# Kernel tuning notes

Measured on AMD Instinct MI355X. Metric: run time of the kernel, lower is better.

The kernel has to match this reference:

```python
import jax, jax.numpy as jnp
import numpy as np

T, H, E, I, K = 2048, 2048, 8, 1408, 2


def setup_inputs() -> dict:
    key = jax.random.key(0)
    k1, k2, k3, k4, k5 = jax.random.split(key, 5)
    s = 0.02
    return {
        "hidden_states": jax.random.normal(k1, (T, H), dtype=jnp.float32),
        "gate_w": jax.random.normal(k2, (E, H), dtype=jnp.float32) * s,   # router weight [n_experts, hidden]
        "w_gate": jax.random.normal(k3, (E, H, I), dtype=jnp.float32) * s,  # per-expert gate_proj
        "w_up": jax.random.normal(k4, (E, H, I), dtype=jnp.float32) * s,    # per-expert up_proj
        "w_down": jax.random.normal(k5, (E, I, H), dtype=jnp.float32) * s,  # per-expert down_proj
        "top_k": K,
    }


def reference(hidden_states, gate_w, w_gate, w_up, w_down, top_k):
    # Router: linear gate -> softmax -> top-k with renormalized weights (DeepSeek-V2 normal MoE)
    logits = hidden_states @ gate_w.T                       # [T, E]
    probs = jax.nn.softmax(logits, axis=-1)                 # [T, E]
    topv, topi = jax.lax.top_k(probs, top_k)                # [T, K]
    topv = topv / jnp.sum(topv, axis=-1, keepdims=True)     # norm_topk_prob
    nt, ne = probs.shape
    # Sparse combine weights [T, E] (zero for unselected experts)
    combine = jnp.zeros((nt, ne), probs.dtype).at[jnp.arange(nt)[:, None], topi].set(topv)
    # Expert MLPs (gated SiLU): down( silu(x @ Wg) * (x @ Wu) )
    g = jnp.einsum('th,ehi->tei', hidden_states, w_gate)    # [T, E, I]
    u = jnp.einsum('th,ehi->tei', hidden_states, w_up)
    a = jax.nn.silu(g) * u
    y = jnp.einsum('tei,eih->teh', a, w_down)               # [T, E, H]
    # Weighted combine over selected experts
    out = jnp.einsum('te,teh->th', combine, y)              # [T, H]
    return out
```

## Files before the change

kernel.cpp:

```cpp
#include <hip/hip_runtime.h>
#include <hip/hip_bf16.h>

#define T_TOK 2048
#define HID   2048
#define NEXP  8
#define INTER 1408

typedef float f32x4 __attribute__((ext_vector_type(4)));
typedef __bf16 bf16x8 __attribute__((ext_vector_type(8)));

__device__ __forceinline__ unsigned pk(__bf16 a, __bf16 b) {
    return (unsigned)__builtin_bit_cast(unsigned short, a) |
           ((unsigned)__builtin_bit_cast(unsigned short, b) << 16);
}

__global__ __launch_bounds__(256)
void router_kernel(const float* __restrict__ hs, const float* __restrict__ gw,
                   int* __restrict__ cnt, int* __restrict__ list,
                   float* __restrict__ wslot)
{
    const int wv = threadIdx.x >> 6, lane = threadIdx.x & 63;
    const int t = blockIdx.x * 4 + wv;
    float acc[8];
#pragma unroll
    for (int e = 0; e < 8; ++e) acc[e] = 0.f;
    const float* xr = hs + (size_t)t * HID;
    for (int it = 0; it < HID / 256; ++it) {
        const int h = it * 256 + lane * 4;
        float4 x = *reinterpret_cast<const float4*>(xr + h);
#pragma unroll
        for (int e = 0; e < 8; ++e) {
            float4 g = *reinterpret_cast<const float4*>(gw + e * HID + h);
            acc[e] += x.x * g.x + x.y * g.y + x.z * g.z + x.w * g.w;
        }
    }
#pragma unroll
    for (int e = 0; e < 8; ++e) {
#pragma unroll
        for (int off = 32; off >= 1; off >>= 1)
            acc[e] += __shfl_xor(acc[e], off, 64);
    }
    if (lane == 0) {
        int b0 = 0, b1 = -1;
        float v0 = -1e30f, v1 = -1e30f;
#pragma unroll
        for (int e = 0; e < 8; ++e) {
            if (acc[e] > v0) { v1 = v0; b1 = b0; v0 = acc[e]; b0 = e; }
            else if (acc[e] > v1) { v1 = acc[e]; b1 = e; }
        }
        float w0 = 1.f / (1.f + __expf(v1 - v0));
        float w1 = 1.f - w0;
        int p0 = atomicAdd(&cnt[b0], 1);
        list[b0 * T_TOK + p0] = 2 * t;
        wslot[2 * t] = w0;
        int p1 = atomicAdd(&cnt[b1], 1);
        list[b1 * T_TOK + p1] = 2 * t + 1;
        wslot[2 * t + 1] = w1;
    }
}

template<int MODE, int K_, int N_>
__global__ __launch_bounds__(256, 2)
void moe_gemm(const float* __restrict__ Asrc, const float* __restrict__ Ball,
              const int* __restrict__ cnt, const int* __restrict__ list,
              const float* __restrict__ wslot, const float* __restrict__ Gbuf,
              float* __restrict__ Obuf)
{
    const int e = blockIdx.z;
    const int cntE = cnt[e];
    const int rb = blockIdx.x * 128;
    if (rb >= cntE) return;
    const int nb = blockIdx.y * 128;
    const int tid = threadIdx.x;
    const int lane = tid & 63;
    const int wv = tid >> 6;
    const int wr = (wv >> 1) * 64, wc = (wv & 1) * 64;
    const int p = lane & 15, kg = lane >> 4;

    __shared__ __align__(16) __bf16 AhL[128 * 40], AlL[128 * 40];
    __shared__ __align__(16) __bf16 BhL[128 * 40], BlL[128 * 40];
    __shared__ int slots[128];

    if (tid < 128) {
        int r = rb + tid;
        slots[tid] = (r < cntE) ? list[e * T_TOK + r] : 0;
    }
    __syncthreads();

    const float* Bsrc = Ball + (size_t)e * K_ * N_;

    f32x4 acc[4][4];
#pragma unroll
    for (int i = 0; i < 4; ++i)
#pragma unroll
        for (int j = 0; j < 4; ++j) acc[i][j] = (f32x4)0.0f;

    for (int kt = 0; kt < K_ / 32; ++kt) {
        const int kb = kt * 32;
#pragma unroll
        for (int pp = 0; pp < 4; ++pp) {
            int idx = tid + pp * 256;
            int row = idx >> 3, c4 = idx & 7;
            int s = slots[row];
            size_t arow = (MODE < 2) ? (size_t)(s >> 1) * HID : (size_t)s * K_;
            float4 v = *reinterpret_cast<const float4*>(Asrc + arow + kb + c4 * 4);
            __bf16 h0 = (__bf16)v.x, h1 = (__bf16)v.y, h2 = (__bf16)v.z, h3 = (__bf16)v.w;
            uint2 hi, lo;
            hi.x = pk(h0, h1); hi.y = pk(h2, h3);
            lo.x = pk((__bf16)(v.x - (float)h0), (__bf16)(v.y - (float)h1));
            lo.y = pk((__bf16)(v.z - (float)h2), (__bf16)(v.w - (float)h3));
            int off = row * 40 + c4 * 4;
            *reinterpret_cast<uint2*>(&AhL[off]) = hi;
            *reinterpret_cast<uint2*>(&AlL[off]) = lo;
        }
        {
            int kblk = tid >> 5, a = tid & 31;
            int k0 = kblk * 4, n0 = a * 4;
            float4 r0 = *reinterpret_cast<const float4*>(Bsrc + (size_t)(kb + k0 + 0) * N_ + nb + n0);
            float4 r1 = *reinterpret_cast<const float4*>(Bsrc + (size_t)(kb + k0 + 1) * N_ + nb + n0);
            float4 r2 = *reinterpret_cast<const float4*>(Bsrc + (size_t)(kb + k0 + 2) * N_ + nb + n0);
            float4 r3 = *reinterpret_cast<const float4*>(Bsrc + (size_t)(kb + k0 + 3) * N_ + nb + n0);
            const float* rr0 = (const float*)&r0;
            const float* rr1 = (const float*)&r1;
            const float* rr2 = (const float*)&r2;
            const float* rr3 = (const float*)&r3;
#pragma unroll
            for (int cc = 0; cc < 4; ++cc) {
                int n = n0 + cc;
                float x0 = rr0[cc], x1 = rr1[cc], x2 = rr2[cc], x3 = rr3[cc];
                __bf16 h0 = (__bf16)x0, h1 = (__bf16)x1, h2 = (__bf16)x2, h3 = (__bf16)x3;
                uint2 hi, lo;
                hi.x = pk(h0, h1); hi.y = pk(h2, h3);
                lo.x = pk((__bf16)(x0 - (float)h0), (__bf16)(x1 - (float)h1));
                lo.y = pk((__bf16)(x2 - (float)h2), (__bf16)(x3 - (float)h3));
                int kx = k0 ^ (((n >> 3) & 3) << 3);
                int off = n * 40 + kx;
                *reinterpret_cast<uint2*>(&BhL[off]) = hi;
                *reinterpret_cast<uint2*>(&BlL[off]) = lo;
            }
        }
        __syncthreads();

        bf16x8 ah[4], al[4], bh[4], bl[4];
#pragma unroll
        for (int mi = 0; mi < 4; ++mi) {
            int off = (wr + mi * 16 + p) * 40 + kg * 8;
            ah[mi] = *reinterpret_cast<const bf16x8*>(&AhL[off]);
            al[mi] = *reinterpret_cast<const bf16x8*>(&AlL[off]);
        }
#pragma unroll
        for (int ni = 0; ni < 4; ++ni) {
            int n = wc + ni * 16 + p;
            int kx = (kg * 8) ^ (((n >> 3) & 3) << 3);
            int off = n * 40 + kx;
            bh[ni] = *reinterpret_cast<const bf16x8*>(&BhL[off]);
            bl[ni] = *reinterpret_cast<const bf16x8*>(&BlL[off]);
        }
#pragma unroll
        for (int mi = 0; mi < 4; ++mi)
#pragma unroll
            for (int ni = 0; ni < 4; ++ni) {
                acc[mi][ni] = __builtin_amdgcn_mfma_f32_16x16x32_bf16(ah[mi], bh[ni], acc[mi][ni], 0, 0, 0);
                acc[mi][ni] = __builtin_amdgcn_mfma_f32_16x16x32_bf16(ah[mi], bl[ni], acc[mi][ni], 0, 0, 0);
                acc[mi][ni] = __builtin_amdgcn_mfma_f32_16x16x32_bf16(al[mi], bh[ni], acc[mi][ni], 0, 0, 0);
            }
        __syncthreads();
    }

#pragma unroll
    for (int mi = 0; mi < 4; ++mi) {
#pragma unroll
        for (int j = 0; j < 4; ++j) {
            int lr = wr + mi * 16 + kg * 4 + j;
            int gr = rb + lr;
            if (gr < cntE) {
                int s = slots[lr];
#pragma unroll
                for (int ni = 0; ni < 4; ++ni) {
                    int col = nb + wc + ni * 16 + p;
                    float v = acc[mi][ni][j];
                    if (MODE == 0) {
                        Obuf[(size_t)s * N_ + col] = v;
                    } else if (MODE == 1) {
                        float g = Gbuf[(size_t)s * N_ + col];
                        float a = g / (1.f + __expf(-g));
                        Obuf[(size_t)s * N_ + col] = a * v;
                    } else {
                        float w = wslot[s];
                        atomicAdd(&Obuf[(size_t)(s >> 1) * N_ + col], v * w);
                    }
                }
            }
        }
    }
}

extern "C" void kernel_launch(void* const* d_in, const int* in_sizes, int n_in,
                              void* d_out, int out_size, void* d_ws, size_t ws_size,
                              hipStream_t stream)
{
    const float* hs = (const float*)d_in[0];
    const float* gw = (const float*)d_in[1];
    const float* wg = (const float*)d_in[2];
    const float* wu = (const float*)d_in[3];
    const float* wd = (const float*)d_in[4];
    float* out = (float*)d_out;

    char* ws = (char*)d_ws;
    int*   cnt   = (int*)(ws);
    int*   list  = (int*)(ws + 256);
    float* wslot = (float*)(ws + 256 + 65536);
    float* G     = (float*)(ws + (1 << 20));
    float* A     = (float*)(ws + (1 << 20) + (size_t)23068672);

    hipMemsetAsync(cnt, 0, 8 * sizeof(int), stream);
    hipMemsetAsync(out, 0, (size_t)out_size * sizeof(float), stream);

    router_kernel<<<T_TOK / 4, 256, 0, stream>>>(hs, gw, cnt, list, wslot);

    moe_gemm<0, 2048, 1408><<<dim3(16, 11, 8), 256, 0, stream>>>(hs, wg, cnt, list, wslot, nullptr, G);
    moe_gemm<1, 2048, 1408><<<dim3(16, 11, 8), 256, 0, stream>>>(hs, wu, cnt, list, wslot, G, A);
    moe_gemm<2, 1408, 2048><<<dim3(16, 16, 8), 256, 0, stream>>>(A, wd, cnt, list, wslot, nullptr, out);
}
```

Baseline: 1.132 ms.

## Fuse gate/up GEMMs, pre-split activations to bf16, prefetch tiles via LDS DMA

Gate and up projections now run in one kernel that computes both accumulators and applies SiLU-multiply in the epilogue, which removes the fp32 G round-trip and one launch. Hidden states are split into bf16 hi/lo once by a new pack kernel, and intermediate activations are stored as bf16 hi/lo. A tiles are then staged into LDS with global_load_lds while the next B tile is loaded into registers during the MFMAs, giving software pipelining. The N tile shrinks to 64 and occupancy hints change. The per-tile B loads are strided scalar column reads, which may be poorly coalesced.

```diff
diff --git a/kernel.cpp b/kernel.cpp
--- a/kernel.cpp
+++ b/kernel.cpp
@@ -8,10 +8,35 @@
 
 typedef float f32x4 __attribute__((ext_vector_type(4)));
 typedef __bf16 bf16x8 __attribute__((ext_vector_type(8)));
-
-__device__ __forceinline__ unsigned pk(__bf16 a, __bf16 b) {
-    return (unsigned)__builtin_bit_cast(unsigned short, a) |
-           ((unsigned)__builtin_bit_cast(unsigned short, b) << 16);
+typedef unsigned int u32;
+
+__device__ __forceinline__ u32 pk(__bf16 a, __bf16 b) {
+    return (u32)__builtin_bit_cast(unsigned short, a) |
+           ((u32)__builtin_bit_cast(unsigned short, b) << 16);
+}
+
+__device__ __forceinline__ void pack8(const float* v, uint4& hi, uint4& lo) {
+    __bf16 h[8];
+#pragma unroll
+    for (int j = 0; j < 8; ++j) h[j] = (__bf16)v[j];
+    hi.x = pk(h[0], h[1]); hi.y = pk(h[2], h[3]);
+    hi.z = pk(h[4], h[5]); hi.w = pk(h[6], h[7]);
+    float r[8];
+#pragma unroll
+    for (int j = 0; j < 8; ++j) r[j] = v[j] - (float)h[j];
+    lo.x = pk((__bf16)r[0], (__bf16)r[1]); lo.y = pk((__bf16)r[2], (__bf16)r[3]);
+    lo.z = pk((__bf16)r[4], (__bf16)r[5]); lo.w = pk((__bf16)r[6], (__bf16)r[7]);
+}
+
+__device__ __forceinline__ void dma16(const __bf16* g, __bf16* ldsWaveBase, int lane) {
+#if __has_builtin(__builtin_amdgcn_global_load_lds)
+    __builtin_amdgcn_global_load_lds(
+        (const __attribute__((address_space(1))) u32*)g,
+        (__attribute__((address_space(3))) u32*)ldsWaveBase, 16, 0, 0);
+#else
+    *reinterpret_cast<bf16x8*>(ldsWaveBase + lane * 8) =
+        *reinterpret_cast<const bf16x8*>(g);
+#endif
 }
 
 __global__ __launch_bounds__(256)
@@ -59,26 +84,37 @@
     }
 }
 
-template<int MODE, int K_, int N_>
-__global__ __launch_bounds__(256, 2)
-void moe_gemm(const float* __restrict__ Asrc, const float* __restrict__ Ball,
-              const int* __restrict__ cnt, const int* __restrict__ list,
-              const float* __restrict__ wslot, const float* __restrict__ Gbuf,
-              float* __restrict__ Obuf)
+__global__ __launch_bounds__(256)
+void pack_x(const float* __restrict__ x, __bf16* __restrict__ xh, __bf16* __restrict__ xl)
+{
+    size_t i = ((size_t)blockIdx.x * 256 + threadIdx.x) * 4;
+    float4 v = *reinterpret_cast<const float4*>(x + i);
+    __bf16 h0 = (__bf16)v.x, h1 = (__bf16)v.y, h2 = (__bf16)v.z, h3 = (__bf16)v.w;
+    uint2 hi, lo;
+    hi.x = pk(h0, h1); hi.y = pk(h2, h3);
+    lo.x = pk((__bf16)(v.x - (float)h0), (__bf16)(v.y - (float)h1));
+    lo.y = pk((__bf16)(v.z - (float)h2), (__bf16)(v.w - (float)h3));
+    *reinterpret_cast<uint2*>(xh + i) = hi;
+    *reinterpret_cast<uint2*>(xl + i) = lo;
+}
+
+__global__ __launch_bounds__(256, 3)
+void moe_gateup(const __bf16* __restrict__ xh, const __bf16* __restrict__ xl,
+                const float* __restrict__ wgAll, const float* __restrict__ wuAll,
+                const int* __restrict__ cnt, const int* __restrict__ list,
+                __bf16* __restrict__ actH, __bf16* __restrict__ actL)
 {
     const int e = blockIdx.z;
     const int cntE = cnt[e];
     const int rb = blockIdx.x * 128;
     if (rb >= cntE) return;
-    const int nb = blockIdx.y * 128;
-    const int tid = threadIdx.x;
-    const int lane = tid & 63;
-    const int wv = tid >> 6;
-    const int wr = (wv >> 1) * 64, wc = (wv & 1) * 64;
+    const int nb = blockIdx.y;
+    const int tid = threadIdx.x, lane = tid & 63, wv = tid >> 6;
+    const int wr = (wv >> 1) * 64, wc = (wv & 1) * 32;
     const int p = lane & 15, kg = lane >> 4;
 
-    __shared__ __align__(16) __bf16 AhL[128 * 40], AlL[128 * 40];
-    __shared__ __align__(16) __bf16 BhL[128 * 40], BlL[128 * 40];
+    __shared__ __bf16 AhL[4096], AlL[4096];
+    __shared__ __bf16 BghL[2048], BglL[2048], BuhL[2048], BulL[2048];
     __shared__ int slots[128];
 
     if (tid < 128) {
@@ -87,112 +123,220 @@
     }
     __syncthreads();
 
-    const float* Bsrc = Ball + (size_t)e * K_ * N_;
-
-    f32x4 acc[4][4];
+    const size_t tok = (size_t)(slots[tid & 127] >> 1);
+    const __bf16* aSrcH = xh + tok * HID + (tid >> 7) * 8;
+    const __bf16* aSrcL = xl + tok * HID + (tid >> 7) * 8;
+    __bf16* aDst0h = &AhL[(wv * 64) * 8];
+    __bf16* aDst1h = &AhL[(256 + wv * 64) * 8];
+    __bf16* aDst0l = &AlL[(wv * 64) * 8];
+    __bf16* aDst1l = &AlL[(256 + wv * 64) * 8];
+
+    const size_t wbase = (size_t)e * HID * INTER + (size_t)((tid >> 6) * 8) * INTER
+                       + (size_t)nb * 64 + (tid & 63);
+    const float* bgSrc = wgAll + wbase;
+    const float* buSrc = wuAll + wbase;
+
+    f32x4 accG[4][2], accU[4][2];
 #pragma unroll
     for (int i = 0; i < 4; ++i)
 #pragma unroll
-        for (int j = 0; j < 4; ++j) acc[i][j] = (f32x4)0.0f;
-
-    for (int kt = 0; kt < K_ / 32; ++kt) {
-        const int kb = kt * 32;
-#pragma unroll
-        for (int pp = 0; pp < 4; ++pp) {
-            int idx = tid + pp * 256;
-            int row = idx >> 3, c4 = idx & 7;
-            int s = slots[row];
-            size_t arow = (MODE < 2) ? (size_t)(s >> 1) * HID : (size_t)s * K_;
-            float4 v = *reinterpret_cast<const float4*>(Asrc + arow + kb + c4 * 4);
-            __bf16 h0 = (__bf16)v.x, h1 = (__bf16)v.y, h2 = (__bf16)v.z, h3 = (__bf16)v.w;
-            uint2 hi, lo;
-            hi.x = pk(h0, h1); hi.y = pk(h2, h3);
-            lo.x = pk((__bf16)(v.x - (float)h0), (__bf16)(v.y - (float)h1));
-            lo.y = pk((__bf16)(v.z - (float)h2), (__bf16)(v.w - (float)h3));
-            int off = row * 40 + c4 * 4;
-            *reinterpret_cast<uint2*>(&AhL[off]) = hi;
-            *reinterpret_cast<uint2*>(&AlL[off]) = lo;
-        }
-        {
-            int kblk = tid >> 5, a = tid & 31;
-            int k0 = kblk * 4, n0 = a * 4;
-            float4 r0 = *reinterpret_cast<const float4*>(Bsrc + (size_t)(kb + k0 + 0) * N_ + nb + n0);
-            float4 r1 = *reinterpret_cast<const float4*>(Bsrc + (size_t)(kb + k0 + 1) * N_ + nb + n0);
-            float4 r2 = *reinterpret_cast<const float4*>(Bsrc + (size_t)(kb + k0 + 2) * N_ + nb + n0);
-            float4 r3 = *reinterpret_cast<const float4*>(Bsrc + (size_t)(kb + k0 + 3) * N_ + nb + n0);
-            const float* rr0 = (const float*)&r0;
-            const float* rr1 = (const float*)&r1;
-            const float* rr2 = (const float*)&r2;
-            const float* rr3 = (const float*)&r3;
-#pragma unroll
-            for (int cc = 0; cc < 4; ++cc) {
-                int n = n0 + cc;
-                float x0 = rr0[cc], x1 = rr1[cc], x2 = rr2[cc], x3 = rr3[cc];
-                __bf16 h0 = (__bf16)x0, h1 = (__bf16)x1, h2 = (__bf16)x2, h3 = (__bf16)x3;
-                uint2 hi, lo;
-                hi.x = pk(h0, h1); hi.y = pk(h2, h3);
-                lo.x = pk((__bf16)(x0 - (float)h0), (__bf16)(x1 - (float)h1));
-                lo.y = pk((__bf16)(x2 - (float)h2), (__bf16)(x3 - (float)h3));
-                int kx = k0 ^ (((n >> 3) & 3) << 3);
-                int off = n * 40 + kx;
-                *reinterpret_cast<uint2*>(&BhL[off]) = hi;
-                *reinterpret_cast<uint2*>(&BlL[off]) = lo;
-            }
-        }
-        __syncthreads();
-
-        bf16x8 ah[4], al[4], bh[4], bl[4];
+        for (int j = 0; j < 2; ++j) { accG[i][j] = (f32x4)0.f; accU[i][j] = (f32x4)0.f; }
+
+    float bg[8], bu[8];
+
+#define LOADB(kb) { \
+    const float* s1_ = bgSrc + (size_t)(kb) * INTER; \
+    const float* s2_ = buSrc + (size_t)(kb) * INTER; \
+    _Pragma("unroll") for (int j = 0; j < 8; ++j) bg[j] = s1_[(size_t)j * INTER]; \
+    _Pragma("unroll") for (int j = 0; j < 8; ++j) bu[j] = s2_[(size_t)j * INTER]; }
+
+#define STAGEA(kb) { \
+    dma16(aSrcH + (kb),      aDst0h, lane); \
+    dma16(aSrcH + (kb) + 16, aDst1h, lane); \
+    dma16(aSrcL + (kb),      aDst0l, lane); \
+    dma16(aSrcL + (kb) + 16, aDst1l, lane); }
+
+#define WRITEB() { \
+    uint4 h_, l_; \
+    pack8(bg, h_, l_); \
+    *reinterpret_cast<uint4*>(&BghL[tid * 8]) = h_; \
+    *reinterpret_cast<uint4*>(&BglL[tid * 8]) = l_; \
+    pack8(bu, h_, l_); \
+    *reinterpret_cast<uint4*>(&BuhL[tid * 8]) = h_; \
+    *reinterpret_cast<uint4*>(&BulL[tid * 8]) = l_; }
+
+    LOADB(0); STAGEA(0); WRITEB();
+    __syncthreads();
+
+    for (int kt = 0; kt < HID / 32; ++kt) {
+        bf16x8 ah[4], al[4], bgh[2], bgl[2], buh[2], bul[2];
 #pragma unroll
         for (int mi = 0; mi < 4; ++mi) {
-            int off = (wr + mi * 16 + p) * 40 + kg * 8;
+            int off = (kg * 128 + wr + mi * 16 + p) * 8;
             ah[mi] = *reinterpret_cast<const bf16x8*>(&AhL[off]);
             al[mi] = *reinterpret_cast<const bf16x8*>(&AlL[off]);
         }
 #pragma unroll
-        for (int ni = 0; ni < 4; ++ni) {
-            int n = wc + ni * 16 + p;
-            int kx = (kg * 8) ^ (((n >> 3) & 3) << 3);
-            int off = n * 40 + kx;
+        for (int ni = 0; ni < 2; ++ni) {
+            int off = (kg * 64 + wc + ni * 16 + p) * 8;
+            bgh[ni] = *reinterpret_cast<const bf16x8*>(&BghL[off]);
+            bgl[ni] = *reinterpret_cast<const bf16x8*>(&BglL[off]);
+            buh[ni] = *reinterpret_cast<const bf16x8*>(&BuhL[off]);
+            bul[ni] = *reinterpret_cast<const bf16x8*>(&BulL[off]);
+        }
+        __syncthreads();
+        const bool more = (kt + 1) < (HID / 32);
+        if (more) { STAGEA((kt + 1) * 32); LOADB((kt + 1) * 32); }
+#pragma unroll
+        for (int mi = 0; mi < 4; ++mi)
+#pragma unroll
+            for (int ni = 0; ni < 2; ++ni) {
+                accG[mi][ni] = __builtin_amdgcn_mfma_f32_16x16x32_bf16(ah[mi], bgh[ni], accG[mi][ni], 0, 0, 0);
+                accG[mi][ni] = __builtin_amdgcn_mfma_f32_16x16x32_bf16(ah[mi], bgl[ni], accG[mi][ni], 0, 0, 0);
+                accG[mi][ni] = __builtin_amdgcn_mfma_f32_16x16x32_bf16(al[mi], bgh[ni], accG[mi][ni], 0, 0, 0);
+                accU[mi][ni] = __builtin_amdgcn_mfma_f32_16x16x32_bf16(ah[mi], buh[ni], accU[mi][ni], 0, 0, 0);
+                accU[mi][ni] = __builtin_amdgcn_mfma_f32_16x16x32_bf16(ah[mi], bul[ni], accU[mi][ni], 0, 0, 0);
+                accU[mi][ni] = __builtin_amdgcn_mfma_f32_16x16x32_bf16(al[mi], buh[ni], accU[mi][ni], 0, 0, 0);
+            }
+        if (more) { WRITEB(); }
+        __syncthreads();
+    }
+#undef LOADB
+#undef STAGEA
+#undef WRITEB
+
+    const size_t nb64 = (size_t)nb * 64;
+#pragma unroll
+    for (int mi = 0; mi < 4; ++mi)
+#pragma unroll
+        for (int j = 0; j < 4; ++j) {
+            int lr = wr + mi * 16 + kg * 4 + j;
+            if (rb + lr < cntE) {
+                size_t rowoff = (size_t)slots[lr] * INTER + nb64;
+#pragma unroll
+                for (int ni = 0; ni < 2; ++ni) {
+                    int col = wc + ni * 16 + p;
+                    float g = accG[mi][ni][j], u = accU[mi][ni][j];
+                    float a = g / (1.f + __expf(-g)) * u;
+                    __bf16 h = (__bf16)a;
+                    actH[rowoff + col] = h;
+                    actL[rowoff + col] = (__bf16)(a - (float)h);
+                }
+            }
+        }
+}
+
+__global__ __launch_bounds__(256, 4)
+void moe_down(const __bf16* __restrict__ actH, const __bf16* __restrict__ actL,
+              const float* __restrict__ wdAll,
+              const int* __restrict__ cnt, const int* __restrict__ list,
+              const float* __restrict__ wslot, float* __restrict__ out)
+{
+    const int e = blockIdx.z;
+    const int cntE = cnt[e];
+    const int rb = blockIdx.x * 128;
+    if (rb >= cntE) return;
+    const int nb = blockIdx.y;
+    const int tid = threadIdx.x, lane = tid & 63, wv = tid >> 6;
+    const int wr = (wv >> 1) * 64, wc = (wv & 1) * 32;
+    const int p = lane & 15, kg = lane >> 4;
+
+    __shared__ __bf16 AhL[4096], AlL[4096];
+    __shared__ __bf16 BhL[2048], BlL[2048];
+    __shared__ int slots[128];
+
+    if (tid < 128) {
+        int r = rb + tid;
+        slots[tid] = (r < cntE) ? list[e * T_TOK + r] : 0;
+    }
+    __syncthreads();
+
+    const __bf16* aSrcH = actH + (size_t)slots[tid & 127] * INTER + (tid >> 7) * 8;
+    const __bf16* aSrcL = actL + (size_t)slots[tid & 127] * INTER + (tid >> 7) * 8;
+    __bf16* aDst0h = &AhL[(wv * 64) * 8];
+    __bf16* aDst1h = &AhL[(256 + wv * 64) * 8];
+    __bf16* aDst0l = &AlL[(wv * 64) * 8];
+    __bf16* aDst1l = &AlL[(256 + wv * 64) * 8];
+
+    const float* bdSrc = wdAll + (size_t)e * INTER * HID
+                       + (size_t)((tid >> 6) * 8) * HID + (size_t)nb * 64 + (tid & 63);
+
+    f32x4 acc[4][2];
+#pragma unroll
+    for (int i = 0; i < 4; ++i)
+#pragma unroll
+        for (int j = 0; j < 2; ++j) acc[i][j] = (f32x4)0.f;
+
+    float bd[8];
+
+#define LOADB(kb) { \
+    const float* s1_ = bdSrc + (size_t)(kb) * HID; \
+    _Pragma("unroll") for (int j = 0; j < 8; ++j) bd[j] = s1_[(size_t)j * HID]; }
+
+#define STAGEA(kb) { \
+    dma16(aSrcH + (kb),      aDst0h, lane); \
+    dma16(aSrcH + (kb) + 16, aDst1h, lane); \
+    dma16(aSrcL + (kb),      aDst0l, lane); \
+    dma16(aSrcL + (kb) + 16, aDst1l, lane); }
+
+#define WRITEB() { \
+    uint4 h_, l_; \
+    pack8(bd, h_, l_); \
+    *reinterpret_cast<uint4*>(&BhL[tid * 8]) = h_; \
+    *reinterpret_cast<uint4*>(&BlL[tid * 8]) = l_; }
+
+    LOADB(0); STAGEA(0); WRITEB();
+    __syncthreads();
+
+    for (int kt = 0; kt < INTER / 32; ++kt) {
+        bf16x8 ah[4], al[4], bh[2], bl[2];
+#pragma unroll
+        for (int mi = 0; mi < 4; ++mi) {
+            int off = (kg * 128 + wr + mi * 16 + p) * 8;
+            ah[mi] = *reinterpret_cast<const bf16x8*>(&AhL[off]);
+            al[mi] = *reinterpret_cast<const bf16x8*>(&AlL[off]);
+        }
+#pragma unroll
+        for (int ni = 0; ni < 2; ++ni) {
+            int off = (kg * 64 + wc + ni * 16 + p) * 8;
             bh[ni] = *reinterpret_cast<const bf16x8*>(&BhL[off]);
             bl[ni] = *reinterpret_cast<const bf16x8*>(&BlL[off]);
         }
+        __syncthreads();
+        const bool more = (kt + 1) < (INTER / 32);
+        if (more) { STAGEA((kt + 1) * 32); LOADB((kt + 1) * 32); }
 #pragma unroll
         for (int mi = 0; mi < 4; ++mi)
 #pragma unroll
-            for (int ni = 0; ni < 4; ++ni) {
+            for (int ni = 0; ni < 2; ++ni) {
                 acc[mi][ni] = __builtin_amdgcn_mfma_f32_16x16x32_bf16(ah[mi], bh[ni], acc[mi][ni], 0, 0, 0);
                 acc[mi][ni] = __builtin_amdgcn_mfma_f32_16x16x32_bf16(ah[mi], bl[ni], acc[mi][ni], 0, 0, 0);
                 acc[mi][ni] = __builtin_amdgcn_mfma_f32_16x16x32_bf16(al[mi], bh[ni], acc[mi][ni], 0, 0, 0);
             }
+        if (more) { WRITEB(); }
         __syncthreads();
     }
-
-#pragma unroll
-    for (int mi = 0; mi < 4; ++mi) {
+#undef LOADB
+#undef STAGEA
+#undef WRITEB
+
+    const size_t nb64 = (size_t)nb * 64;
+#pragma unroll
+    for (int mi = 0; mi < 4; ++mi)
 #pragma unroll
         for (int j = 0; j < 4; ++j) {
             int lr = wr + mi * 16 + kg * 4 + j;
-            int gr = rb + lr;
-            if (gr < cntE) {
+            if (rb + lr < cntE) {
                 int s = slots[lr];
-#pragma unroll
-                for (int ni = 0; ni < 4; ++ni) {
-                    int col = nb + wc + ni * 16 + p;
-                    float v = acc[mi][ni][j];
-                    if (MODE == 0) {
-                        Obuf[(size_t)s * N_ + col] = v;
-                    } else if (MODE == 1) {
-                        float g = Gbuf[(size_t)s * N_ + col];
-                        float a = g / (1.f + __expf(-g));
-                        Obuf[(size_t)s * N_ + col] = a * v;
-                    } else {
-                        float w = wslot[s];
-                        atomicAdd(&Obuf[(size_t)(s >> 1) * N_ + col], v * w);
-                    }
+                float w = wslot[s];
+                size_t rowoff = (size_t)(s >> 1) * HID + nb64;
+#pragma unroll
+                for (int ni = 0; ni < 2; ++ni) {
+                    int col = wc + ni * 16 + p;
+                    atomicAdd(&out[rowoff + col], acc[mi][ni][j] * w);
                 }
             }
         }
-    }
 }
 
 extern "C" void kernel_launch(void* const* d_in, const int* in_sizes, int n_in,
@@ -207,18 +351,20 @@
     float* out = (float*)d_out;
 
     char* ws = (char*)d_ws;
-    int*   cnt   = (int*)(ws);
-    int*   list  = (int*)(ws + 256);
-    float* wslot = (float*)(ws + 256 + 65536);
-    float* G     = (float*)(ws + (1 << 20));
-    float* A     = (float*)(ws + (1 << 20) + (size_t)23068672);
+    int*    cnt   = (int*)(ws);
+    int*    list  = (int*)(ws + 256);
+    float*  wslot = (float*)(ws + 256 + 65536);
+    __bf16* Xh    = (__bf16*)(ws + 1048576);
+    __bf16* Xl    = (__bf16*)(ws + 1048576 + 8388608);
+    __bf16* actH  = (__bf16*)(ws + 1048576 + 2 * 8388608);
+    __bf16* actL  = (__bf16*)(ws + 1048576 + 2 * 8388608 + 11534336);
 
     hipMemsetAsync(cnt, 0, 8 * sizeof(int), stream);
     hipMemsetAsync(out, 0, (size_t)out_size * sizeof(float), stream);
 
+    pack_x<<<(T_TOK * HID / 4) / 256, 256, 0, stream>>>(hs, Xh, Xl);
     router_kernel<<<T_TOK / 4, 256, 0, stream>>>(hs, gw, cnt, list, wslot);
 
-    moe_gemm<0, 2048, 1408><<<dim3(16, 11, 8), 256, 0, stream>>>(hs, wg, cnt, list, wslot, nullptr, G);
-    moe_gemm<1, 2048, 1408><<<dim3(16, 11, 8), 256, 0, stream>>>(hs, wu, cnt, list, wslot, G, A);
-    moe_gemm<2, 1408, 2048><<<dim3(16, 16, 8), 256, 0, stream>>>(A, wd, cnt, list, wslot, nullptr, out);
-}
+    moe_gateup<<<dim3(16, INTER / 64, NEXP), 256, 0, stream>>>(Xh, Xl, wg, wu, cnt, list, actH, actL);
+    moe_down<<<dim3(16, HID / 64, NEXP), 256, 0, stream>>>(actH, actL, wd, cnt, list, wslot, out);
+}
```

Measured after the change: 1.460 ms. 1.29x slower.
